# Optimization experiments

Measured on AMD Instinct MI355X. Metric: run time of the kernel, lower is better.

The kernel has to match this reference:

```python
import jax, jax.numpy as jnp
import numpy as np

N, E, H, L, G = 100000, 1600000, 128, 2, 64
MID = H // 2


def setup_inputs() -> dict:
    key = jax.random.key(0)
    ks = jax.random.split(key, 24)
    s = 1.0 / np.sqrt(H)
    inp = {
        "x": jax.random.normal(ks[0], (N, 1), jnp.float32),
        "edge_index": jax.random.randint(ks[1], (2, E), 0, N, jnp.int64),
        "edge_attr": jax.random.uniform(ks[2], (E, 1), jnp.float32),
        "batch": jnp.sort(jax.random.randint(ks[3], (N,), 0, G, jnp.int64)),
        # encoders
        "enc_w": jax.random.normal(ks[4], (1, H), jnp.float32),
        "enc_b": jnp.zeros((H,), jnp.float32),
        "edge_w": jax.random.normal(ks[5], (1, H), jnp.float32),
        "edge_b": jnp.zeros((H,), jnp.float32),
        # per-layer GINE params (stacked over L layers)
        "eps": jnp.zeros((L,), jnp.float32),
        "mlp_w1": jax.random.normal(ks[6], (L, H, H), jnp.float32) * s,
        "mlp_b1": jnp.zeros((L, H), jnp.float32),
        "mlp_w2": jax.random.normal(ks[7], (L, H, H), jnp.float32) * s,
        "mlp_b2": jnp.zeros((L, H), jnp.float32),
        # BatchNorm1d (eval mode: running stats)
        "bn_gamma": jnp.ones((L, H), jnp.float32),
        "bn_beta": jnp.zeros((L, H), jnp.float32),
        "bn_mean": jax.random.normal(ks[8], (L, H), jnp.float32) * 0.1,
        "bn_var": jnp.ones((L, H), jnp.float32),
        # classifier (binary head)
        "cls_w1": jax.random.normal(ks[9], (H, MID), jnp.float32) * s,
        "cls_b1": jnp.zeros((MID,), jnp.float32),
        "cls_w2": jax.random.normal(ks[10], (MID, 1), jnp.float32) * s,
        "cls_b2": jnp.zeros((1,), jnp.float32),
    }
    return inp


def reference(x, edge_index, edge_attr, batch, enc_w, enc_b, edge_w, edge_b,
              eps, mlp_w1, mlp_b1, mlp_w2, mlp_b2,
              bn_gamma, bn_beta, bn_mean, bn_var,
              cls_w1, cls_b1, cls_w2, cls_b2):
    BN_EPS = 1e-5
    n = x.shape[0]
    h = x @ enc_w + enc_b              # [N,H]
    e = edge_attr @ edge_w + edge_b    # [E,H]
    src, dst = edge_index[0], edge_index[1]
    for l in range(L):
        # GINEConv: sum_j relu(h_j + e_ji), then nn((1+eps)h_i + aggr)
        msg = jax.nn.relu(h[src] + e)                       # [E,H] edge gather
        aggr = jax.ops.segment_sum(msg, dst, num_segments=n)  # scatter-add
        z = (1.0 + eps[l]) * h + aggr
        z = jax.nn.relu(z @ mlp_w1[l] + mlp_b1[l]) @ mlp_w2[l] + mlp_b2[l]
        # BatchNorm1d (eval) + ReLU; dropout is identity in eval
        z = (z - bn_mean[l]) * jax.lax.rsqrt(bn_var[l] + BN_EPS) * bn_gamma[l] + bn_beta[l]
        h = jax.nn.relu(z)
    # global_mean_pool over graph assignment
    sums = jax.ops.segment_sum(h, batch, num_segments=G)
    cnts = jax.ops.segment_sum(jnp.ones((n, 1), h.dtype), batch, num_segments=G)
    g = sums / jnp.maximum(cnts, 1.0)
    g = jax.nn.relu(g @ cls_w1 + cls_b1)
    out = jax.nn.sigmoid(g @ cls_w2 + cls_b2)
    return out.squeeze(-1)  # [G], num_classes == 2
```

## Files before the change

### kernel.cpp

```cpp
#include <hip/hip_runtime.h>
#include <hip/hip_bf16.h>

#define H 128
#define NGRAPH 64
#define NLAYERS 2
#define TMM 64
#define TP 136
#define BSH 8
#define MAXB 512

typedef short short8 __attribute__((ext_vector_type(8)));
typedef float floatx4 __attribute__((ext_vector_type(4)));
typedef float floatx2 __attribute__((ext_vector_type(2)));

static __device__ __forceinline__ unsigned short f2bf(float v) {
    __hip_bfloat16 b = __float2bfloat16(v);
    return *(unsigned short*)&b;
}
static __device__ __forceinline__ float bf2f(unsigned short u) {
    return __uint_as_float(((unsigned int)u) << 16);
}
static __device__ __forceinline__ int pack4_fp8(float a, float b, float c, float d) {
    int p = __builtin_amdgcn_cvt_pk_fp8_f32(a, b, 0, false);
    p = __builtin_amdgcn_cvt_pk_fp8_f32(c, d, p, true);
    return p;
}

__global__ void enc_kernel(const float* __restrict__ x, const float* __restrict__ w,
                           const float* __restrict__ b, const float* __restrict__ eb,
                           unsigned short* __restrict__ h,
                           unsigned char* __restrict__ h8, int n) {
    int t = blockIdx.x * blockDim.x + threadIdx.x;
    int i = t >> 5;
    int c = (t & 31) << 2;
    if (i >= n) return;
    float xv = x[i];
    float4 wv = *(const float4*)(w + c);
    float4 bv = *(const float4*)(b + c);
    float4 ev = *(const float4*)(eb + c);
    float4 o;
    o.x = xv * wv.x + bv.x;
    o.y = xv * wv.y + bv.y;
    o.z = xv * wv.z + bv.z;
    o.w = xv * wv.w + bv.w;
    ushort4 ob;
    ob.x = f2bf(o.x); ob.y = f2bf(o.y); ob.z = f2bf(o.z); ob.w = f2bf(o.w);
    *(ushort4*)(h + (size_t)i * H + c) = ob;
    *(int*)(h8 + (size_t)i * H + c) =
        pack4_fp8(o.x + ev.x, o.y + ev.y, o.z + ev.z, o.w + ev.w);
}

__global__ void prep_kernel(const float* __restrict__ w1, const float* __restrict__ w2,
                            unsigned short* __restrict__ w1f, unsigned short* __restrict__ w2f,
                            const float* __restrict__ b2, const float* __restrict__ g,
                            const float* __restrict__ bt, const float* __restrict__ mn,
                            const float* __restrict__ vr,
                            float* __restrict__ scb, float* __restrict__ shb) {
    int idx = blockIdx.x * blockDim.x + threadIdx.x;
    int l = idx >> 14;
    int r = idx & 16383;
    int nn = r >> 7;
    int kk = r & 127;
    int ct = nn >> 4, m = nn & 15;
    int kbi = kk >> 5, q = (kk >> 3) & 3, j = kk & 7;
    int fo = l * 16384 + ct * 2048 + kbi * 512 + (q * 16 + m) * 8 + j;
    w1f[fo] = f2bf(w1[(size_t)l * 16384 + kk * 128 + nn]);
    w2f[fo] = f2bf(w2[(size_t)l * 16384 + kk * 128 + nn]);
    if (idx < NLAYERS * H) {
        float sc = g[idx] * rsqrtf(vr[idx] + 1e-5f);
        scb[idx] = sc;
        shb[idx] = (b2[idx] - mn[idx]) * sc + bt[idx];
    }
}

__global__ void hist_kernel(const int* __restrict__ ei, int* __restrict__ deg, int ne) {
    int e = blockIdx.x * blockDim.x + threadIdx.x;
    if (e >= ne) return;
    atomicAdd(&deg[ei[ne + e]], 1);
}

__global__ __launch_bounds__(256) void scan1_kernel(const int* __restrict__ deg,
                                                    int* __restrict__ start,
                                                    int* __restrict__ bsum, int n) {
    __shared__ int wsum[4];
    const int t = threadIdx.x;
    const int lane = t & 63;
    const int wid = t >> 6;
    const int base = blockIdx.x * 1024 + t * 4;
    int4 v = make_int4(0, 0, 0, 0);
    if (base + 3 < n) v = *(const int4*)(deg + base);
    else {
        if (base + 0 < n) v.x = deg[base + 0];
        if (base + 1 < n) v.y = deg[base + 1];
        if (base + 2 < n) v.z = deg[base + 2];
    }
    int s = v.x + v.y + v.z + v.w;
    int incl = s;
    #pragma unroll
    for (int off = 1; off < 64; off <<= 1) {
        int u = __shfl_up(incl, off, 64);
        if (lane >= off) incl += u;
    }
    if (lane == 63) wsum[wid] = incl;
    __syncthreads();
    int woff = 0;
    #pragma unroll
    for (int k = 0; k < 4; ++k) if (k < wid) woff += wsum[k];
    int excl = woff + incl - s;
    int4 o;
    o.x = excl;
    o.y = o.x + v.x;
    o.z = o.y + v.y;
    o.w = o.z + v.z;
    if (base + 3 < n) *(int4*)(start + base) = o;
    else {
        if (base + 0 < n) start[base + 0] = o.x;
        if (base + 1 < n) start[base + 1] = o.y;
        if (base + 2 < n) start[base + 2] = o.z;
    }
    if (t == 255) bsum[blockIdx.x] = woff + incl;
}

__global__ __launch_bounds__(256) void scan2_kernel(const int* __restrict__ bsum,
                                                    int* __restrict__ bscan,
                                                    int* __restrict__ start, int nb, int n) {
    __shared__ int wsum[4];
    const int t = threadIdx.x;
    const int lane = t & 63;
    const int wid = t >> 6;
    int v = (t < nb) ? bsum[t] : 0;
    int incl = v;
    #pragma unroll
    for (int off = 1; off < 64; off <<= 1) {
        int u = __shfl_up(incl, off, 64);
        if (lane >= off) incl += u;
    }
    if (lane == 63) wsum[wid] = incl;
    __syncthreads();
    int woff = 0;
    #pragma unroll
    for (int k = 0; k < 4; ++k) if (k < wid) woff += wsum[k];
    if (t < nb) bscan[t] = woff + incl - v;
    if (t == 255) start[n] = woff + incl;
}

__global__ void scan3_kernel(int* __restrict__ start, const int* __restrict__ bscan, int n) {
    int i = blockIdx.x * blockDim.x + threadIdx.x;
    if (i < n) start[i] += bscan[i >> 10];
}

__global__ __launch_bounds__(256) void binA_kernel(
    const int* __restrict__ ei, const float* __restrict__ ea,
    const int* __restrict__ start, int* __restrict__ bcursor,
    int2* __restrict__ sedge2, int ne, int n, int nbuck) {
    __shared__ int hist[MAXB];
    __shared__ int gpos[MAXB];
    const int t = threadIdx.x;
    const int e0 = blockIdx.x * 4096;
    for (int k = t; k < MAXB; k += 256) hist[k] = 0;
    __syncthreads();
    int dsts[16];
    #pragma unroll
    for (int k = 0; k < 16; ++k) {
        int e = e0 + k * 256 + t;
        int d = (e < ne) ? ei[ne + e] : -1;
        dsts[k] = d;
        if (d >= 0) atomicAdd(&hist[d >> BSH], 1);
    }
    __syncthreads();
    for (int b = t; b < nbuck; b += 256) {
        int c = hist[b];
        gpos[b] = (c > 0) ? (start[b << BSH] + atomicAdd(&bcursor[b], c)) : 0;
    }
    __syncthreads();
    for (int k = t; k < MAXB; k += 256) hist[k] = 0;
    __syncthreads();
    #pragma unroll
    for (int k = 0; k < 16; ++k) {
        int d = dsts[k];
        if (d >= 0) {
            int e = e0 + k * 256 + t;
            int b = d >> BSH;
            int idx = atomicAdd(&hist[b], 1);
            int2 p;
            p.x = ei[e];
            p.y = ((int)f2bf(ea[e]) << 16) | (d & ((1 << BSH) - 1));
            sedge2[gpos[b] + idx] = p;
        }
    }
}

__global__ __launch_bounds__(256) void binB_kernel(
    const int2* __restrict__ sedge2, const int* __restrict__ start,
    int2* __restrict__ sedge, int n) {
    __shared__ int lcur[1 << BSH];
    const int node0 = blockIdx.x << BSH;
    const int t = threadIdx.x;
    lcur[t] = 0;
    __syncthreads();
    int s0 = start[node0];
    int s1 = start[min(node0 + (1 << BSH), n)];
    for (int i = s0 + t; i < s1; i += 256) {
        int2 p = sedge2[i];
        int ld = p.y & ((1 << BSH) - 1);
        int idx = atomicAdd(&lcur[ld], 1);
        p.y = (int)((unsigned)p.y & 0xffff0000u);
        sedge[start[node0 + ld] + idx] = p;
    }
}

__global__ __launch_bounds__(256) void aggregate_kernel(
    const unsigned short* __restrict__ h, const unsigned char* __restrict__ h8,
    const int* __restrict__ start, const int2* __restrict__ sedge,
    const float* __restrict__ ew,
    const float* __restrict__ epsp, int layer,
    unsigned short* __restrict__ z, int n) {
    int node = (blockIdx.x * blockDim.x + threadIdx.x) >> 6;
    int lane = threadIdx.x & 63;
    if (node >= n) return;
    const unsigned c = (unsigned)lane << 1;
    float2 wv = *(const float2*)(ew + c);
    float2 acc = make_float2(0.f, 0.f);
    int s0 = start[node], s1 = start[node + 1];
    int j = s0;
    for (; j + 16 <= s1; j += 16) {
        int2 e[16];
        unsigned short v8[16];
        #pragma unroll
        for (int k = 0; k < 16; ++k) e[k] = sedge[j + k];
        #pragma unroll
        for (int k = 0; k < 16; ++k)
            v8[k] = *(const unsigned short*)(h8 + (((unsigned)e[k].x << 7) + c));
        #pragma unroll
        for (int k = 0; k < 16; ++k) {
            float a = __int_as_float(e[k].y);
            floatx2 hv = __builtin_amdgcn_cvt_pk_f32_fp8((int)v8[k], false);
            acc.x += fmaxf(fmaf(a, wv.x, hv.x), 0.f);
            acc.y += fmaxf(fmaf(a, wv.y, hv.y), 0.f);
        }
    }
    if (j + 8 <= s1) {
        int2 e[8];
        unsigned short v8[8];
        #pragma unroll
        for (int k = 0; k < 8; ++k) e[k] = sedge[j + k];
        #pragma unroll
        for (int k = 0; k < 8; ++k)
            v8[k] = *(const unsigned short*)(h8 + (((unsigned)e[k].x << 7) + c));
        #pragma unroll
        for (int k = 0; k < 8; ++k) {
            float a = __int_as_float(e[k].y);
            floatx2 hv = __builtin_amdgcn_cvt_pk_f32_fp8((int)v8[k], false);
            acc.x += fmaxf(fmaf(a, wv.x, hv.x), 0.f);
            acc.y += fmaxf(fmaf(a, wv.y, hv.y), 0.f);
        }
        j += 8;
    }
    if (j < s1) {
        int2 e[8];
        unsigned short v8[8];
        #pragma unroll
        for (int k = 0; k < 8; ++k) {
            int idx = j + k;
            e[k] = sedge[idx < s1 ? idx : (s1 - 1)];
        }
        #pragma unroll
        for (int k = 0; k < 8; ++k)
            v8[k] = *(const unsigned short*)(h8 + (((unsigned)e[k].x << 7) + c));
        #pragma unroll
        for (int k = 0; k < 8; ++k) {
            float valid = (j + k < s1) ? 1.f : 0.f;
            float a = __int_as_float(e[k].y);
            floatx2 hv = __builtin_amdgcn_cvt_pk_f32_fp8((int)v8[k], false);
            acc.x += valid * fmaxf(fmaf(a, wv.x, hv.x), 0.f);
            acc.y += valid * fmaxf(fmaf(a, wv.y, hv.y), 0.f);
        }
    }
    float ev = 1.0f + epsp[layer];
    ushort2 hv = *(const ushort2*)(h + (size_t)node * H + c);
    ushort2 p;
    p.x = f2bf(fmaf(ev, bf2f(hv.x), acc.x));
    p.y = f2bf(fmaf(ev, bf2f(hv.y), acc.y));
    *(ushort2*)(z + (size_t)node * H + c) = p;
}

__global__ __launch_bounds__(256) void mfma_mlp_kernel(
    unsigned short* __restrict__ h, const unsigned short* __restrict__ z,
    const unsigned short* __restrict__ w1f, const float* __restrict__ b1,
    const unsigned short* __restrict__ w2f,
    const float* __restrict__ scb, const float* __restrict__ shb,
    unsigned char* __restrict__ h8out, const float* __restrict__ eb, int n) {
    __shared__ unsigned short zs[4][16 * TP];
    __shared__ unsigned short ts[4][16 * TP];
    const int tid = threadIdx.x;
    const int wid = tid >> 6;
    const int lane = tid & 63;
    const int m = lane & 15;
    const int q = lane >> 4;
    const int row0 = blockIdx.x * TMM + wid * 16;

    unsigned short* zw = zs[wid];
    {
        const unsigned short* zg = z + (size_t)row0 * H;
        #pragma unroll
        for (int i = 0; i < 4; ++i) {
            int idx = i * 64 + lane;
            int r = idx >> 4;
            int c8 = (idx & 15) << 3;
            short8 v = (short8)(0);
            if (row0 + r < n) v = *(const short8*)(zg + r * H + c8);
            *(short8*)(zw + r * TP + c8) = v;
        }
    }

    floatx4 acc[8];
    #pragma unroll
    for (int ct = 0; ct < 8; ++ct) acc[ct] = (floatx4)(0.f);

    #pragma unroll
    for (int kbi = 0; kbi < 4; ++kbi) {
        short8 a = *(const short8*)(zw + m * TP + kbi * 32 + q * 8);
        #pragma unroll
        for (int ct = 0; ct < 8; ++ct) {
            short8 b = *(const short8*)(w1f + ct * 2048 + kbi * 512 + lane * 8);
            acc[ct] = __builtin_amdgcn_mfma_f32_16x16x32_bf16(a, b, acc[ct], 0, 0, 0);
        }
    }
    unsigned short* tw = ts[wid];
    #pragma unroll
    for (int ct = 0; ct < 8; ++ct) {
        float bb = b1[ct * 16 + m];
        #pragma unroll
        for (int r = 0; r < 4; ++r) {
            float v = fmaxf(acc[ct][r] + bb, 0.f);
            tw[(q * 4 + r) * TP + ct * 16 + m] = f2bf(v);
        }
    }

    floatx4 acc2[8];
    #pragma unroll
    for (int ct = 0; ct < 8; ++ct) acc2[ct] = (floatx4)(0.f);

    #pragma unroll
    for (int kbi = 0; kbi < 4; ++kbi) {
        short8 a = *(const short8*)(tw + m * TP + kbi * 32 + q * 8);
        #pragma unroll
        for (int ct = 0; ct < 8; ++ct) {
            short8 b = *(const short8*)(w2f + ct * 2048 + kbi * 512 + lane * 8);
            acc2[ct] = __builtin_amdgcn_mfma_f32_16x16x32_bf16(a, b, acc2[ct], 0, 0, 0);
        }
    }
    #pragma unroll
    for (int ct = 0; ct < 8; ++ct) {
        int col = ct * 16 + m;
        float scv = scb[col];
        float shv = shb[col];
        #pragma unroll
        for (int r = 0; r < 4; ++r) {
            float v = fmaxf(fmaf(acc2[ct][r], scv, shv), 0.f);
            zw[(q * 4 + r) * TP + col] = f2bf(v);
        }
    }
    {
        unsigned short* hg = h + (size_t)row0 * H;
        #pragma unroll
        for (int i = 0; i < 4; ++i) {
            int idx = i * 64 + lane;
            int r = idx >> 4;
            int c8 = (idx & 15) << 3;
            if (row0 + r < n)
                *(short8*)(hg + r * H + c8) = *(const short8*)(zw + r * TP + c8);
        }
    }
    if (h8out) {
        unsigned char* h8g = h8out + (size_t)row0 * H;
        #pragma unroll
        for (int i = 0; i < 4; ++i) {
            int idx = i * 64 + lane;
            int r = idx >> 4;
            int c8 = (idx & 15) << 3;
            if (row0 + r < n) {
                const unsigned short* src = zw + r * TP + c8;
                float4 e0 = *(const float4*)(eb + c8);
                float4 e1 = *(const float4*)(eb + c8 + 4);
                int2 pk;
                pk.x = pack4_fp8(bf2f(src[0]) + e0.x, bf2f(src[1]) + e0.y,
                                 bf2f(src[2]) + e0.z, bf2f(src[3]) + e0.w);
                pk.y = pack4_fp8(bf2f(src[4]) + e1.x, bf2f(src[5]) + e1.y,
                                 bf2f(src[6]) + e1.z, bf2f(src[7]) + e1.w);
                *(int2*)(h8g + r * H + c8) = pk;
            }
        }
    }
}

__global__ void gbound_kernel(const int* __restrict__ batch, int* __restrict__ gstart, int n) {
    int i = blockIdx.x * blockDim.x + threadIdx.x;
    if (i >= n) return;
    int b = batch[i];
    if (i == 0) {
        for (int g = 0; g <= b; ++g) gstart[g] = 0;
    } else {
        int p = batch[i - 1];
        for (int g = p + 1; g <= b; ++g) gstart[g] = i;
    }
    if (i == n - 1) {
        for (int g = b + 1; g <= NGRAPH; ++g) gstart[g] = n;
    }
}

__global__ __launch_bounds__(256) void pool_kernel(const unsigned short* __restrict__ h,
                                                   const int* __restrict__ gstart,
                                                   float* __restrict__ sums) {
    __shared__ float4 buf[8][32];
    const int g = blockIdx.x;
    const int split = blockIdx.y;
    const int t = threadIdx.x;
    const int c32 = t & 31;
    const int c = c32 << 2;
    const int r = t >> 5;
    int s0 = gstart[g], s1 = gstart[g + 1];
    int len = s1 - s0;
    int chunk = (len + 7) >> 3;
    int a = s0 + split * chunk;
    int b = min(a + chunk, s1);
    float4 acc = make_float4(0.f, 0.f, 0.f, 0.f);
    for (int i = a + r; i < b; i += 8) {
        ushort4 v = *(const ushort4*)(h + (size_t)i * H + c);
        acc.x += bf2f(v.x); acc.y += bf2f(v.y); acc.z += bf2f(v.z); acc.w += bf2f(v.w);
    }
    buf[r][c32] = acc;
    __syncthreads();
    if (r == 0) {
        float4 s = buf[0][c32];
        #pragma unroll
        for (int k = 1; k < 8; ++k) {
            float4 v = buf[k][c32];
            s.x += v.x; s.y += v.y; s.z += v.z; s.w += v.w;
        }
        float* sp = sums + (size_t)g * H + c;
        atomicAdd(sp + 0, s.x);
        atomicAdd(sp + 1, s.y);
        atomicAdd(sp + 2, s.z);
        atomicAdd(sp + 3, s.w);
    }
}

__global__ void cls_kernel(const float* __restrict__ sums, const int* __restrict__ gstart,
                           const float* __restrict__ w1, const float* __restrict__ b1,
                           const float* __restrict__ w2, const float* __restrict__ b2,
                           float* __restrict__ out) {
    int g = blockIdx.x;
    int m = threadIdx.x;
    float cnt = (float)(gstart[g + 1] - gstart[g]);
    float inv = 1.0f / fmaxf(cnt, 1.0f);
    float acc = 0.f;
    for (int k = 0; k < H; ++k) {
        float gk = sums[(size_t)g * H + k] * inv;
        acc += gk * w1[(size_t)k * 64 + m];
    }
    float tm = fmaxf(acc + b1[m], 0.f);
    float p = tm * w2[m];
    #pragma unroll
    for (int off = 32; off > 0; off >>= 1) p += __shfl_down(p, off, 64);
    if (m == 0) out[g] = 1.f / (1.f + expf(-(p + b2[0])));
}

extern "C" void kernel_launch(void* const* d_in, const int* in_sizes, int n_in,
                              void* d_out, int out_size, void* d_ws, size_t ws_size,
                              hipStream_t stream) {
    const float* x      = (const float*)d_in[0];
    const int*   ei     = (const int*)d_in[1];
    const float* ea     = (const float*)d_in[2];
    const int*   batch  = (const int*)d_in[3];
    const float* enc_w  = (const float*)d_in[4];
    const float* enc_b  = (const float*)d_in[5];
    const float* edge_w = (const float*)d_in[6];
    const float* edge_b = (const float*)d_in[7];
    const float* eps    = (const float*)d_in[8];
    const float* mlp_w1 = (const float*)d_in[9];
    const float* mlp_b1 = (const float*)d_in[10];
    const float* mlp_w2 = (const float*)d_in[11];
    const float* mlp_b2 = (const float*)d_in[12];
    const float* bn_g   = (const float*)d_in[13];
    const float* bn_b   = (const float*)d_in[14];
    const float* bn_m   = (const float*)d_in[15];
    const float* bn_v   = (const float*)d_in[16];
    const float* cls_w1 = (const float*)d_in[17];
    const float* cls_b1 = (const float*)d_in[18];
    const float* cls_w2 = (const float*)d_in[19];
    const float* cls_b2 = (const float*)d_in[20];
    float* out = (float*)d_out;

    const int n = in_sizes[0];
    const int ne = in_sizes[2];
    const int nb = (n + 1023) / 1024;
    const int nbuck = (n + (1 << BSH) - 1) >> BSH;

    unsigned short* hb  = (unsigned short*)d_ws;
    unsigned short* zb  = hb + (size_t)n * H;
    unsigned char* h8   = (unsigned char*)(zb + (size_t)n * H);
    float* sums         = (float*)(h8 + (size_t)n * H);
    int*   deg          = (int*)(sums + (size_t)NGRAPH * H);
    int*   bcursor      = deg + n;
    int*   gstart       = bcursor + MAXB;
    int*   start        = gstart + NGRAPH + 4;
    int*   bsum         = start + n + 4;
    int*   bscan        = bsum + 256;
    float* scb          = (float*)(bscan + 256);
    float* shb          = scb + NLAYERS * H;
    unsigned short* w1f = (unsigned short*)(shb + NLAYERS * H);
    unsigned short* w2f = w1f + 2 * 16384;
    int2*  sedge2       = (int2*)(w2f + 2 * 16384);
    int2*  sedge        = sedge2 + ne;

    hipMemsetAsync(sums, 0, ((size_t)NGRAPH * H + n + MAXB) * sizeof(int), stream);

    prep_kernel<<<128, 256, 0, stream>>>(mlp_w1, mlp_w2, w1f, w2f,
                                         mlp_b2, bn_g, bn_b, bn_m, bn_v, scb, shb);

    hist_kernel<<<(ne + 255) / 256, 256, 0, stream>>>(ei, deg, ne);
    scan1_kernel<<<nb, 256, 0, stream>>>(deg, start, bsum, n);
    scan2_kernel<<<1, 256, 0, stream>>>(bsum, bscan, start, nb, n);
    scan3_kernel<<<(n + 255) / 256, 256, 0, stream>>>(start, bscan, n);
    binA_kernel<<<(ne + 4095) / 4096, 256, 0, stream>>>(ei, ea, start, bcursor, sedge2, ne, n, nbuck);
    binB_kernel<<<nbuck, 256, 0, stream>>>(sedge2, start, sedge, n);

    gbound_kernel<<<(n + 255) / 256, 256, 0, stream>>>(batch, gstart, n);

    {
        int threads = n * 32;
        enc_kernel<<<(threads + 255) / 256, 256, 0, stream>>>(x, enc_w, enc_b, edge_b, hb, h8, n);
    }

    for (int l = 0; l < NLAYERS; ++l) {
        {
            int threads = n * 64;
            aggregate_kernel<<<(threads + 255) / 256, 256, 0, stream>>>(
                hb, h8, start, sedge, edge_w, eps, l, zb, n);
        }
        mfma_mlp_kernel<<<(n + TMM - 1) / TMM, 256, 0, stream>>>(
            hb, zb,
            w1f + (size_t)l * 16384, mlp_b1 + (size_t)l * H,
            w2f + (size_t)l * 16384,
            scb + (size_t)l * H, shb + (size_t)l * H,
            (l == 0) ? h8 : (unsigned char*)nullptr, edge_b, n);
    }

    pool_kernel<<<dim3(NGRAPH, 8), 256, 0, stream>>>(hb, gstart, sums);
    cls_kernel<<<NGRAPH, 64, 0, stream>>>(sums, gstart, cls_w1, cls_b1, cls_w2, cls_b2, out);
}
```

Measured before the change: 422.4 us.

## Replace per-node degree histogram and 3-pass scan with bucket-level histogram

Drops the per-node global atomic degree histogram and the three-kernel node-level prefix scan. It now computes a per-bucket (256-node) histogram with shared-memory atomics, scans the roughly 391 buckets in one block, and derives per-node CSR offsets inside binB through a local histogram and scan over each bucket's edges. This removes 1.6M global atomics and two kernel launches. In exchange, binB reads sedge2 twice.

```diff
diff --git a/kernel.cpp b/kernel.cpp
--- a/kernel.cpp
+++ b/kernel.cpp
@@ -73,28 +73,37 @@
     }
 }
 
-__global__ void hist_kernel(const int* __restrict__ ei, int* __restrict__ deg, int ne) {
-    int e = blockIdx.x * blockDim.x + threadIdx.x;
-    if (e >= ne) return;
-    atomicAdd(&deg[ei[ne + e]], 1);
-}
-
-__global__ __launch_bounds__(256) void scan1_kernel(const int* __restrict__ deg,
+__global__ __launch_bounds__(256) void histB_kernel(const int* __restrict__ ei,
+                                                    int* __restrict__ bcnt, int ne) {
+    __shared__ int hist[MAXB];
+    const int t = threadIdx.x;
+    const int e0 = blockIdx.x * 4096;
+    for (int k = t; k < MAXB; k += 256) hist[k] = 0;
+    __syncthreads();
+    #pragma unroll
+    for (int k = 0; k < 16; ++k) {
+        int e = e0 + k * 256 + t;
+        if (e < ne) atomicAdd(&hist[ei[ne + e] >> BSH], 1);
+    }
+    __syncthreads();
+    for (int b = t; b < MAXB; b += 256) {
+        int c = hist[b];
+        if (c > 0) atomicAdd(&bcnt[b], c);
+    }
+}
+
+__global__ __launch_bounds__(256) void scanB_kernel(const int* __restrict__ bcnt,
+                                                    int* __restrict__ bstart,
                                                     int* __restrict__ start,
-                                                    int* __restrict__ bsum, int n) {
+                                                    int nbuck, int n, int ne) {
     __shared__ int wsum[4];
     const int t = threadIdx.x;
     const int lane = t & 63;
     const int wid = t >> 6;
-    const int base = blockIdx.x * 1024 + t * 4;
-    int4 v = make_int4(0, 0, 0, 0);
-    if (base + 3 < n) v = *(const int4*)(deg + base);
-    else {
-        if (base + 0 < n) v.x = deg[base + 0];
-        if (base + 1 < n) v.y = deg[base + 1];
-        if (base + 2 < n) v.z = deg[base + 2];
-    }
-    int s = v.x + v.y + v.z + v.w;
+    int i0 = 2 * t, i1 = 2 * t + 1;
+    int v0 = (i0 < nbuck) ? bcnt[i0] : 0;
+    int v1 = (i1 < nbuck) ? bcnt[i1] : 0;
+    int s = v0 + v1;
     int incl = s;
     #pragma unroll
     for (int off = 1; off < 64; off <<= 1) {
@@ -107,52 +116,15 @@
     #pragma unroll
     for (int k = 0; k < 4; ++k) if (k < wid) woff += wsum[k];
     int excl = woff + incl - s;
-    int4 o;
-    o.x = excl;
-    o.y = o.x + v.x;
-    o.z = o.y + v.y;
-    o.w = o.z + v.z;
-    if (base + 3 < n) *(int4*)(start + base) = o;
-    else {
-        if (base + 0 < n) start[base + 0] = o.x;
-        if (base + 1 < n) start[base + 1] = o.y;
-        if (base + 2 < n) start[base + 2] = o.z;
-    }
-    if (t == 255) bsum[blockIdx.x] = woff + incl;
-}
-
-__global__ __launch_bounds__(256) void scan2_kernel(const int* __restrict__ bsum,
-                                                    int* __restrict__ bscan,
-                                                    int* __restrict__ start, int nb, int n) {
-    __shared__ int wsum[4];
-    const int t = threadIdx.x;
-    const int lane = t & 63;
-    const int wid = t >> 6;
-    int v = (t < nb) ? bsum[t] : 0;
-    int incl = v;
-    #pragma unroll
-    for (int off = 1; off < 64; off <<= 1) {
-        int u = __shfl_up(incl, off, 64);
-        if (lane >= off) incl += u;
-    }
-    if (lane == 63) wsum[wid] = incl;
-    __syncthreads();
-    int woff = 0;
-    #pragma unroll
-    for (int k = 0; k < 4; ++k) if (k < wid) woff += wsum[k];
-    if (t < nb) bscan[t] = woff + incl - v;
-    if (t == 255) start[n] = woff + incl;
-}
-
-__global__ void scan3_kernel(int* __restrict__ start, const int* __restrict__ bscan, int n) {
-    int i = blockIdx.x * blockDim.x + threadIdx.x;
-    if (i < n) start[i] += bscan[i >> 10];
+    if (i0 < nbuck) bstart[i0] = excl;
+    if (i1 < nbuck) bstart[i1] = excl + v0;
+    if (t == 0) { bstart[nbuck] = ne; start[n] = ne; }
 }
 
 __global__ __launch_bounds__(256) void binA_kernel(
     const int* __restrict__ ei, const float* __restrict__ ea,
-    const int* __restrict__ start, int* __restrict__ bcursor,
-    int2* __restrict__ sedge2, int ne, int n, int nbuck) {
+    const int* __restrict__ bstart, int* __restrict__ bcursor,
+    int2* __restrict__ sedge2, int ne, int nbuck) {
     __shared__ int hist[MAXB];
     __shared__ int gpos[MAXB];
     const int t = threadIdx.x;
@@ -170,7 +142,7 @@
     __syncthreads();
     for (int b = t; b < nbuck; b += 256) {
         int c = hist[b];
-        gpos[b] = (c > 0) ? (start[b << BSH] + atomicAdd(&bcursor[b], c)) : 0;
+        gpos[b] = (c > 0) ? (bstart[b] + atomicAdd(&bcursor[b], c)) : 0;
     }
     __syncthreads();
     for (int k = t; k < MAXB; k += 256) hist[k] = 0;
@@ -191,21 +163,45 @@
 }
 
 __global__ __launch_bounds__(256) void binB_kernel(
-    const int2* __restrict__ sedge2, const int* __restrict__ start,
-    int2* __restrict__ sedge, int n) {
-    __shared__ int lcur[1 << BSH];
+    const int2* __restrict__ sedge2, const int* __restrict__ bstart,
+    int2* __restrict__ sedge, int* __restrict__ start, int n) {
+    __shared__ int nhist[1 << BSH];
+    __shared__ int nstart_s[1 << BSH];
+    __shared__ int wsum[4];
     const int node0 = blockIdx.x << BSH;
     const int t = threadIdx.x;
-    lcur[t] = 0;
-    __syncthreads();
-    int s0 = start[node0];
-    int s1 = start[min(node0 + (1 << BSH), n)];
+    const int lane = t & 63;
+    const int wid = t >> 6;
+    nhist[t] = 0;
+    __syncthreads();
+    int s0 = bstart[blockIdx.x];
+    int s1 = bstart[blockIdx.x + 1];
+    for (int i = s0 + t; i < s1; i += 256)
+        atomicAdd(&nhist[sedge2[i].y & ((1 << BSH) - 1)], 1);
+    __syncthreads();
+    int v = nhist[t];
+    int incl = v;
+    #pragma unroll
+    for (int off = 1; off < 64; off <<= 1) {
+        int u = __shfl_up(incl, off, 64);
+        if (lane >= off) incl += u;
+    }
+    if (lane == 63) wsum[wid] = incl;
+    __syncthreads();
+    int woff = 0;
+    #pragma unroll
+    for (int k = 0; k < 4; ++k) if (k < wid) woff += wsum[k];
+    int excl = woff + incl - v;
+    nstart_s[t] = excl;
+    if (node0 + t < n) start[node0 + t] = s0 + excl;
+    nhist[t] = 0;
+    __syncthreads();
     for (int i = s0 + t; i < s1; i += 256) {
         int2 p = sedge2[i];
         int ld = p.y & ((1 << BSH) - 1);
-        int idx = atomicAdd(&lcur[ld], 1);
+        int idx = atomicAdd(&nhist[ld], 1);
         p.y = (int)((unsigned)p.y & 0xffff0000u);
-        sedge[start[node0 + ld] + idx] = p;
+        sedge[s0 + nstart_s[ld] + idx] = p;
     }
 }
 
@@ -494,37 +490,33 @@
 
     const int n = in_sizes[0];
     const int ne = in_sizes[2];
-    const int nb = (n + 1023) / 1024;
     const int nbuck = (n + (1 << BSH) - 1) >> BSH;
 
     unsigned short* hb  = (unsigned short*)d_ws;
     unsigned short* zb  = hb + (size_t)n * H;
     unsigned char* h8   = (unsigned char*)(zb + (size_t)n * H);
     float* sums         = (float*)(h8 + (size_t)n * H);
-    int*   deg          = (int*)(sums + (size_t)NGRAPH * H);
-    int*   bcursor      = deg + n;
-    int*   gstart       = bcursor + MAXB;
+    int*   bcnt         = (int*)(sums + (size_t)NGRAPH * H);
+    int*   bcursor      = bcnt + MAXB;
+    int*   bstart       = bcursor + MAXB;
+    int*   gstart       = bstart + MAXB + 4;
     int*   start        = gstart + NGRAPH + 4;
-    int*   bsum         = start + n + 4;
-    int*   bscan        = bsum + 256;
-    float* scb          = (float*)(bscan + 256);
+    float* scb          = (float*)(start + n + 4);
     float* shb          = scb + NLAYERS * H;
     unsigned short* w1f = (unsigned short*)(shb + NLAYERS * H);
     unsigned short* w2f = w1f + 2 * 16384;
     int2*  sedge2       = (int2*)(w2f + 2 * 16384);
     int2*  sedge        = sedge2 + ne;
 
-    hipMemsetAsync(sums, 0, ((size_t)NGRAPH * H + n + MAXB) * sizeof(int), stream);
+    hipMemsetAsync(sums, 0, ((size_t)NGRAPH * H + 2 * MAXB) * sizeof(int), stream);
 
     prep_kernel<<<128, 256, 0, stream>>>(mlp_w1, mlp_w2, w1f, w2f,
                                          mlp_b2, bn_g, bn_b, bn_m, bn_v, scb, shb);
 
-    hist_kernel<<<(ne + 255) / 256, 256, 0, stream>>>(ei, deg, ne);
-    scan1_kernel<<<nb, 256, 0, stream>>>(deg, start, bsum, n);
-    scan2_kernel<<<1, 256, 0, stream>>>(bsum, bscan, start, nb, n);
-    scan3_kernel<<<(n + 255) / 256, 256, 0, stream>>>(start, bscan, n);
-    binA_kernel<<<(ne + 4095) / 4096, 256, 0, stream>>>(ei, ea, start, bcursor, sedge2, ne, n, nbuck);
-    binB_kernel<<<nbuck, 256, 0, stream>>>(sedge2, start, sedge, n);
+    histB_kernel<<<(ne + 4095) / 4096, 256, 0, stream>>>(ei, bcnt, ne);
+    scanB_kernel<<<1, 256, 0, stream>>>(bcnt, bstart, start, nbuck, n, ne);
+    binA_kernel<<<(ne + 4095) / 4096, 256, 0, stream>>>(ei, ea, bstart, bcursor, sedge2, ne, nbuck);
+    binB_kernel<<<nbuck, 256, 0, stream>>>(sedge2, bstart, sedge, start, n);
 
     gbound_kernel<<<(n + 255) / 256, 256, 0, stream>>>(batch, gstart, n);
 
```

Result: faster. 365.5 us (median of 2 runs) (-13.5%).
